# Performance work log

Hardware: AMD Instinct MI355X
Metric: run time of the kernel (lower is better)

The kernel has to match this reference:

```python
import jax, jax.numpy as jnp
import numpy as np

_EPS = 1e-08
SEG = 1024
HOP = 256
PAD = SEG // 2

# periodic Hann window, matching torch.hann_window(SEG) (periodic=True default)
_WINDOW = 0.5 * (1.0 - np.cos(2.0 * np.pi * np.arange(SEG) / SEG))


def setup_inputs() -> dict:
    key = jax.random.key(0)
    k1, k2 = jax.random.split(key)
    B, T = 32, 480000
    estimate = jax.random.normal(k1, (B, T), dtype=jnp.float32)
    target = jax.random.normal(k2, (B, T), dtype=jnp.float32)
    return {"estimate": estimate, "target": target}


def _frame(x):
    # x: [B, T_padded] -> [B, n_frames, SEG] overlapping frames (hop=HOP)
    n_frames = (x.shape[1] - SEG) // HOP + 1
    idx = np.arange(n_frames)[:, None] * HOP + np.arange(SEG)[None, :]
    return x[:, idx]


def reference(estimate, target):
    # zero-mean per utterance
    tgt = target - jnp.mean(target, axis=1, keepdims=True)
    est = estimate - jnp.mean(estimate, axis=1, keepdims=True)
    # centering: reflect-pad SEG//2 on both sides
    tgt = jnp.pad(tgt, ((0, 0), (PAD, PAD)), mode="reflect")
    est = jnp.pad(est, ((0, 0), (PAD, PAD)), mode="reflect")
    # overlapping frames + Hann windowing
    w = jnp.asarray(_WINDOW, dtype=tgt.dtype)  # [SEG]
    T_f = _frame(tgt) * w  # [B, F, SEG]
    E_f = _frame(est) * w  # [B, F, SEG]
    # SI-SDR per segment
    dot = jnp.sum(E_f * T_f, axis=2, keepdims=True)
    s_target_energy = jnp.sum(T_f * T_f, axis=2, keepdims=True) + _EPS
    scaled_target = dot * T_f / s_target_energy
    e_noise = E_f - scaled_target
    ratio = jnp.sum(scaled_target * scaled_target, axis=2) / (
        jnp.sum(e_noise * e_noise, axis=2) + _EPS
    )
    losses = -10.0 * jnp.log10(ratio + _EPS)  # [B, F]
    return losses
```

## Files before the change

### kernel.cpp

```cpp
#include <hip/hip_runtime.h>

#define NB 32
#define TLEN 480000
#define NF 1876
#define FR 4
#define WPR 469
#define NWAVE (WPR * NB)
#define WTHREADS 256

template <int CTRL>
__device__ __forceinline__ float dpp_add(float x) {
    int y = __builtin_amdgcn_update_dpp(0, __float_as_int(x), CTRL, 0xF, 0xF, true);
    return x + __int_as_float(y);
}

__device__ __forceinline__ float wave_reduce(float s) {
    s = dpp_add<0xB1>(s);
    s = dpp_add<0x4E>(s);
    s = dpp_add<0x124>(s);
    s = dpp_add<0x128>(s);
    s += __shfl_xor(s, 16);
    s += __shfl_xor(s, 32);
    return s;
}

__device__ __forceinline__ float f4c(const float4& v, int j) {
    return j == 0 ? v.x : (j == 1 ? v.y : (j == 2 ? v.z : v.w));
}

__device__ __forceinline__ float w2fast(float p) {
    float w = 0.5f - 0.5f * __cosf(p * (6.28318530717958647692f / 1024.0f));
    return w * w;
}

__global__ __launch_bounds__(WTHREADS) void seg_frames(
    const float* __restrict__ est, const float* __restrict__ tgt,
    float* __restrict__ ws_part, float* __restrict__ ws_bs)
{
    const int tid  = threadIdx.x;
    const int lane = tid & 63;
    const int wave = tid >> 6;

    const int gw0 = (blockIdx.x & 7) * (NWAVE / 8) + (blockIdx.x >> 3) * 4;
    const int gw  = gw0 + wave;
    const int b   = gw / WPR;
    const int wv  = gw % WPR;
    const int fb  = wv * FR;

    const float* erow = est + (size_t)b * TLEN;
    const float* trow = tgt + (size_t)b * TLEN;

    float pe = 0.f, pt = 0.f;

    if (fb >= 4 && fb <= 1868) {
        const float4* e4 = (const float4*)erow;
        const float4* t4 = (const float4*)trow;

        float4 E[7], T[7];
#pragma unroll
        for (int m = 0; m < 7; ++m) {
            int g = 64 * (fb + m) - 128 + lane;
            E[m] = e4[g];
            T[m] = t4[g];
        }
        __builtin_amdgcn_sched_barrier(0);

        float w2v[4][4];
#pragma unroll
        for (int q = 0; q < 4; ++q)
#pragma unroll
            for (int j = 0; j < 4; ++j)
                w2v[q][j] = w2fast((float)(256 * q + 4 * lane + j));

        float acc[4][5];
#pragma unroll
        for (int i = 0; i < 4; ++i)
#pragma unroll
            for (int s5 = 0; s5 < 5; ++s5) acc[i][s5] = 0.f;

#pragma unroll
        for (int m = 0; m < 7; ++m) {
            float4 ev4 = E[m], tv4 = T[m];
#pragma unroll
            for (int j = 0; j < 4; ++j) {
                float e = f4c(ev4, j), t = f4c(tv4, j);
                float et = e * t, tt2 = t * t, ee2 = e * e;
#pragma unroll
                for (int i = 0; i < 4; ++i) {
                    if (m - i < 0 || m - i > 3) continue;
                    float w2 = w2v[m - i][j];
                    acc[i][0] = fmaf(w2, et,  acc[i][0]);
                    acc[i][1] = fmaf(w2, tt2, acc[i][1]);
                    acc[i][2] = fmaf(w2, ee2, acc[i][2]);
                    acc[i][3] = fmaf(w2, e,   acc[i][3]);
                    acc[i][4] = fmaf(w2, t,   acc[i][4]);
                }
            }
            if (m < 4) {
                pe += (ev4.x + ev4.y) + (ev4.z + ev4.w);
                pt += (tv4.x + tv4.y) + (tv4.z + tv4.w);
            }
        }

#pragma unroll
        for (int i = 0; i < 4; ++i) {
            float s0 = wave_reduce(acc[i][0]);
            float s1 = wave_reduce(acc[i][1]);
            float s2 = wave_reduce(acc[i][2]);
            float s3 = wave_reduce(acc[i][3]);
            float s4 = wave_reduce(acc[i][4]);
            if (lane == 0) {
                float* p = ws_part + (size_t)(b * NF + fb + i) * 5;
                p[0] = s0; p[1] = s1; p[2] = s2; p[3] = s3; p[4] = s4;
            }
        }
    } else {
        int nfr = NF - fb;
        if (nfr > FR) nfr = FR;

        float w2v[4][4];
#pragma unroll
        for (int q = 0; q < 4; ++q)
#pragma unroll
            for (int j = 0; j < 4; ++j)
                w2v[q][j] = w2fast((float)(256 * q + 4 * lane + j));

        for (int i = 0; i < nfr; ++i) {
            int f = fb + i;
            float s_et = 0.f, s_tt = 0.f, s_ee = 0.f, s_e = 0.f, s_t = 0.f;
#pragma unroll
            for (int q = 0; q < 4; ++q)
#pragma unroll
                for (int j = 0; j < 4; ++j) {
                    int s = 256 * f - 512 + 256 * q + 4 * lane + j;
                    int idx = s < 0 ? -s : (s >= TLEN ? 2 * (TLEN - 1) - s : s);
                    float ev = erow[idx], tv = trow[idx];
                    float w2 = w2v[q][j];
                    float et = ev * tv;
                    s_et = fmaf(w2, et,      s_et);
                    s_tt = fmaf(w2, tv * tv, s_tt);
                    s_ee = fmaf(w2, ev * ev, s_ee);
                    s_e  = fmaf(w2, ev, s_e);
                    s_t  = fmaf(w2, tv, s_t);
                }
            s_et = wave_reduce(s_et);
            s_tt = wave_reduce(s_tt);
            s_ee = wave_reduce(s_ee);
            s_e  = wave_reduce(s_e);
            s_t  = wave_reduce(s_t);
            if (lane == 0) {
                float* p = ws_part + (size_t)(b * NF + f) * 5;
                p[0] = s_et; p[1] = s_tt; p[2] = s_ee; p[3] = s_e; p[4] = s_t;
            }
        }

        const float4* e4 = (const float4*)erow;
        const float4* t4 = (const float4*)trow;
        if (fb == 0) {
#pragma unroll
            for (int k = 0; k < 2; ++k) {
                float4 ev4 = e4[lane + 64 * k];
                float4 tv4 = t4[lane + 64 * k];
                pe += (ev4.x + ev4.y) + (ev4.z + ev4.w);
                pt += (tv4.x + tv4.y) + (tv4.z + tv4.w);
            }
        } else {
#pragma unroll
            for (int k = 0; k < 5; ++k) {
                int g = 119680 + lane + 64 * k;
                float4 ev4 = e4[g];
                float4 tv4 = t4[g];
                pe += (ev4.x + ev4.y) + (ev4.z + ev4.w);
                pt += (tv4.x + tv4.y) + (tv4.z + tv4.w);
            }
        }
    }

    pe = wave_reduce(pe);
    pt = wave_reduce(pt);
    if (lane == 0) {
        ws_bs[(0 * NB + b) * WPR + wv] = pe;
        ws_bs[(1 * NB + b) * WPR + wv] = pt;
    }
}

__global__ __launch_bounds__(WTHREADS) void seg_final(
    const float* __restrict__ ws_part, const float* __restrict__ ws_bs,
    float* __restrict__ out)
{
    const int tid  = threadIdx.x;
    const int lane = tid & 63;
    const int wave = tid >> 6;
    const int idx0 = blockIdx.x * WTHREADS;

    int b0 = idx0 / NF;
    int ilast = idx0 + WTHREADS - 1;
    if (ilast > NB * NF - 1) ilast = NB * NF - 1;
    int b1 = ilast / NF;

    __shared__ float smean[4];
    {
        int sig = wave & 1;
        int row = (wave >> 1) ? b1 : b0;
        const float* pbs = ws_bs + (size_t)(sig * NB + row) * WPR;
        float s = 0.f;
        for (int c = lane; c < WPR; c += 64) s += pbs[c];
        s = wave_reduce(s);
        if (lane == 0) smean[wave] = s * (1.0f / (float)TLEN);
    }
    __syncthreads();

    int idx = idx0 + tid;
    if (idx >= NB * NF) return;
    int b = idx / NF;
    int which = (b == b0) ? 0 : 1;
    float me = smean[which * 2 + 0];
    float mt = smean[which * 2 + 1];

    const float* p = ws_part + (size_t)idx * 5;
    float S_et = p[0], S_tt = p[1], S_ee = p[2], S_e = p[3], S_t = p[4];
    const float W2 = 384.0f;

    float dot = S_et - mt * S_e - me * S_t + me * mt * W2;
    float tt  = S_tt - 2.0f * mt * S_t + mt * mt * W2;
    float ee  = S_ee - 2.0f * me * S_e + me * me * W2;

    float a     = dot / (tt + 1e-8f);
    float st2   = a * a * tt;
    float en2   = ee - 2.0f * a * dot + st2;
    float ratio = st2 / (en2 + 1e-8f);
    out[idx] = -10.0f * log10f(ratio + 1e-8f);
}

extern "C" void kernel_launch(void* const* d_in, const int* in_sizes, int n_in,
                              void* d_out, int out_size, void* d_ws, size_t ws_size,
                              hipStream_t stream)
{
    const float* est = (const float*)d_in[0];
    const float* tgt = (const float*)d_in[1];
    float* out = (float*)d_out;

    float* ws      = (float*)d_ws;
    float* ws_part = ws;
    float* ws_bs   = ws_part + (size_t)NB * NF * 5;

    seg_frames<<<NWAVE / 4, WTHREADS, 0, stream>>>(est, tgt, ws_part, ws_bs);
    dim3 grid2((NB * NF + WTHREADS - 1) / WTHREADS);
    seg_final<<<grid2, WTHREADS, 0, stream>>>(ws_part, ws_bs, out);
}
```

Baseline: 34.40 us.

## Load each hop block once per wave and split frame partials across two buffers

Each wave now reads only its own 4 hop-blocks (4 float4 per lane instead of 7) and adds each block's contributions to the 7 frames that overlap it. Partial sums for frames shared with the neighbouring wave go into separate lo/hi workspace arrays, which the final kernel adds together. This removes the redundant overlapped global loads. The window values come from one sin/cos pair using Hann symmetry, and the wave reduction uses DPP row broadcasts plus readlane in place of shuffles. In exchange each wave does more reductions and stores (7 frames instead of 4), and the final kernel reads twice as much workspace.

Result: slower. 35.09 us (+2.0%).

```diff
diff --git a/kernel.cpp b/kernel.cpp
--- a/kernel.cpp
+++ b/kernel.cpp
@@ -3,8 +3,7 @@
 #define NB 32
 #define TLEN 480000
 #define NF 1876
-#define FR 4
-#define WPR 469
+#define WPR 470
 #define NWAVE (WPR * NB)
 #define WTHREADS 256
 
@@ -19,23 +18,19 @@
     s = dpp_add<0x4E>(s);
     s = dpp_add<0x124>(s);
     s = dpp_add<0x128>(s);
-    s += __shfl_xor(s, 16);
-    s += __shfl_xor(s, 32);
-    return s;
+    s = dpp_add<0x142>(s);
+    s = dpp_add<0x143>(s);
+    return __int_as_float(__builtin_amdgcn_readlane(__float_as_int(s), 63));
 }
 
 __device__ __forceinline__ float f4c(const float4& v, int j) {
     return j == 0 ? v.x : (j == 1 ? v.y : (j == 2 ? v.z : v.w));
 }
 
-__device__ __forceinline__ float w2fast(float p) {
-    float w = 0.5f - 0.5f * __cosf(p * (6.28318530717958647692f / 1024.0f));
-    return w * w;
-}
-
 __global__ __launch_bounds__(WTHREADS) void seg_frames(
     const float* __restrict__ est, const float* __restrict__ tgt,
-    float* __restrict__ ws_part, float* __restrict__ ws_bs)
+    float* __restrict__ ws_lo, float* __restrict__ ws_hi,
+    float* __restrict__ ws_bs)
 {
     const int tid  = threadIdx.x;
     const int lane = tid & 63;
@@ -45,134 +40,109 @@
     const int gw  = gw0 + wave;
     const int b   = gw / WPR;
     const int wv  = gw % WPR;
-    const int fb  = wv * FR;
 
     const float* erow = est + (size_t)b * TLEN;
     const float* trow = tgt + (size_t)b * TLEN;
 
+    float w2v[4][4];
+#pragma unroll
+    for (int j = 0; j < 4; ++j) {
+        float ang = (6.28318530717958647692f / 1024.0f) * (float)(4 * lane + j);
+        float c = __cosf(ang), s = __sinf(ang);
+        float w0 = 0.5f - 0.5f * c;
+        float w1 = 0.5f + 0.5f * s;
+        float w2_ = 0.5f + 0.5f * c;
+        float w3 = 0.5f - 0.5f * s;
+        w2v[0][j] = w0 * w0;
+        w2v[1][j] = w1 * w1;
+        w2v[2][j] = w2_ * w2_;
+        w2v[3][j] = w3 * w3;
+    }
+
+    float acc[7][5];
+#pragma unroll
+    for (int df = 0; df < 7; ++df)
+#pragma unroll
+        for (int s5 = 0; s5 < 5; ++s5) acc[df][s5] = 0.f;
+
     float pe = 0.f, pt = 0.f;
 
-    if (fb >= 4 && fb <= 1868) {
+    if (wv >= 1 && wv <= 468) {
         const float4* e4 = (const float4*)erow;
         const float4* t4 = (const float4*)trow;
 
-        float4 E[7], T[7];
-#pragma unroll
-        for (int m = 0; m < 7; ++m) {
-            int g = 64 * (fb + m) - 128 + lane;
-            E[m] = e4[g];
-            T[m] = t4[g];
+        float4 E[4], T[4];
+#pragma unroll
+        for (int u = 0; u < 4; ++u) {
+            int g4 = 64 * (4 * wv - 2 + u) + lane;
+            E[u] = e4[g4];
+            T[u] = t4[g4];
         }
         __builtin_amdgcn_sched_barrier(0);
 
-        float w2v[4][4];
-#pragma unroll
-        for (int q = 0; q < 4; ++q)
-#pragma unroll
-            for (int j = 0; j < 4; ++j)
-                w2v[q][j] = w2fast((float)(256 * q + 4 * lane + j));
-
-        float acc[4][5];
-#pragma unroll
-        for (int i = 0; i < 4; ++i)
-#pragma unroll
-            for (int s5 = 0; s5 < 5; ++s5) acc[i][s5] = 0.f;
-
-#pragma unroll
-        for (int m = 0; m < 7; ++m) {
-            float4 ev4 = E[m], tv4 = T[m];
+#pragma unroll
+        for (int u = 0; u < 4; ++u) {
+            float4 ev4 = E[u], tv4 = T[u];
 #pragma unroll
             for (int j = 0; j < 4; ++j) {
                 float e = f4c(ev4, j), t = f4c(tv4, j);
                 float et = e * t, tt2 = t * t, ee2 = e * e;
 #pragma unroll
-                for (int i = 0; i < 4; ++i) {
-                    if (m - i < 0 || m - i > 3) continue;
-                    float w2 = w2v[m - i][j];
-                    acc[i][0] = fmaf(w2, et,  acc[i][0]);
-                    acc[i][1] = fmaf(w2, tt2, acc[i][1]);
-                    acc[i][2] = fmaf(w2, ee2, acc[i][2]);
-                    acc[i][3] = fmaf(w2, e,   acc[i][3]);
-                    acc[i][4] = fmaf(w2, t,   acc[i][4]);
+                for (int q = 0; q < 4; ++q) {
+                    const int df = u - q + 3;
+                    float w2 = w2v[q][j];
+                    acc[df][0] = fmaf(w2, et,  acc[df][0]);
+                    acc[df][1] = fmaf(w2, tt2, acc[df][1]);
+                    acc[df][2] = fmaf(w2, ee2, acc[df][2]);
+                    acc[df][3] = fmaf(w2, e,   acc[df][3]);
+                    acc[df][4] = fmaf(w2, t,   acc[df][4]);
                 }
             }
-            if (m < 4) {
-                pe += (ev4.x + ev4.y) + (ev4.z + ev4.w);
-                pt += (tv4.x + tv4.y) + (tv4.z + tv4.w);
+            pe += (ev4.x + ev4.y) + (ev4.z + ev4.w);
+            pt += (tv4.x + tv4.y) + (tv4.z + tv4.w);
+        }
+    } else {
+#pragma unroll
+        for (int u = 0; u < 4; ++u) {
+            int g = 4 * wv - 2 + u;
+            bool ownmean = (wv == 0) ? (u >= 2) : (u == 0);
+#pragma unroll
+            for (int j = 0; j < 4; ++j) {
+                int s = 256 * g + 4 * lane + j;
+                int idx = s < 0 ? -s : (s >= TLEN ? 2 * (TLEN - 1) - s : s);
+                float e = erow[idx], t = trow[idx];
+                float et = e * t, tt2 = t * t, ee2 = e * e;
+#pragma unroll
+                for (int q = 0; q < 4; ++q) {
+                    const int df = u - q + 3;
+                    float w2 = w2v[q][j];
+                    acc[df][0] = fmaf(w2, et,  acc[df][0]);
+                    acc[df][1] = fmaf(w2, tt2, acc[df][1]);
+                    acc[df][2] = fmaf(w2, ee2, acc[df][2]);
+                    acc[df][3] = fmaf(w2, e,   acc[df][3]);
+                    acc[df][4] = fmaf(w2, t,   acc[df][4]);
+                }
+                if (ownmean) { pe += e; pt += t; }
             }
         }
-
-#pragma unroll
-        for (int i = 0; i < 4; ++i) {
-            float s0 = wave_reduce(acc[i][0]);
-            float s1 = wave_reduce(acc[i][1]);
-            float s2 = wave_reduce(acc[i][2]);
-            float s3 = wave_reduce(acc[i][3]);
-            float s4 = wave_reduce(acc[i][4]);
-            if (lane == 0) {
-                float* p = ws_part + (size_t)(b * NF + fb + i) * 5;
-                p[0] = s0; p[1] = s1; p[2] = s2; p[3] = s3; p[4] = s4;
-            }
-        }
-    } else {
-        int nfr = NF - fb;
-        if (nfr > FR) nfr = FR;
-
-        float w2v[4][4];
-#pragma unroll
-        for (int q = 0; q < 4; ++q)
-#pragma unroll
-            for (int j = 0; j < 4; ++j)
-                w2v[q][j] = w2fast((float)(256 * q + 4 * lane + j));
-
-        for (int i = 0; i < nfr; ++i) {
-            int f = fb + i;
-            float s_et = 0.f, s_tt = 0.f, s_ee = 0.f, s_e = 0.f, s_t = 0.f;
-#pragma unroll
-            for (int q = 0; q < 4; ++q)
-#pragma unroll
-                for (int j = 0; j < 4; ++j) {
-                    int s = 256 * f - 512 + 256 * q + 4 * lane + j;
-                    int idx = s < 0 ? -s : (s >= TLEN ? 2 * (TLEN - 1) - s : s);
-                    float ev = erow[idx], tv = trow[idx];
-                    float w2 = w2v[q][j];
-                    float et = ev * tv;
-                    s_et = fmaf(w2, et,      s_et);
-                    s_tt = fmaf(w2, tv * tv, s_tt);
-                    s_ee = fmaf(w2, ev * ev, s_ee);
-                    s_e  = fmaf(w2, ev, s_e);
-                    s_t  = fmaf(w2, tv, s_t);
-                }
-            s_et = wave_reduce(s_et);
-            s_tt = wave_reduce(s_tt);
-            s_ee = wave_reduce(s_ee);
-            s_e  = wave_reduce(s_e);
-            s_t  = wave_reduce(s_t);
-            if (lane == 0) {
-                float* p = ws_part + (size_t)(b * NF + f) * 5;
-                p[0] = s_et; p[1] = s_tt; p[2] = s_ee; p[3] = s_e; p[4] = s_t;
-            }
-        }
-
-        const float4* e4 = (const float4*)erow;
-        const float4* t4 = (const float4*)trow;
-        if (fb == 0) {
-#pragma unroll
-            for (int k = 0; k < 2; ++k) {
-                float4 ev4 = e4[lane + 64 * k];
-                float4 tv4 = t4[lane + 64 * k];
-                pe += (ev4.x + ev4.y) + (ev4.z + ev4.w);
-                pt += (tv4.x + tv4.y) + (tv4.z + tv4.w);
-            }
-        } else {
-#pragma unroll
-            for (int k = 0; k < 5; ++k) {
-                int g = 119680 + lane + 64 * k;
-                float4 ev4 = e4[g];
-                float4 tv4 = t4[g];
-                pe += (ev4.x + ev4.y) + (ev4.z + ev4.w);
-                pt += (tv4.x + tv4.y) + (tv4.z + tv4.w);
-            }
+    }
+
+#pragma unroll
+    for (int df = 0; df < 7; ++df) {
+        const int f = 4 * wv + df - 3;
+        if (f >= 0 && f < NF) {
+            float r0 = wave_reduce(acc[df][0]);
+            float r1 = wave_reduce(acc[df][1]);
+            float r2 = wave_reduce(acc[df][2]);
+            float r3 = wave_reduce(acc[df][3]);
+            float r4 = wave_reduce(acc[df][4]);
+            float v = r0;
+            v = (lane == 1) ? r1 : v;
+            v = (lane == 2) ? r2 : v;
+            v = (lane == 3) ? r3 : v;
+            v = (lane == 4) ? r4 : v;
+            float* dst = (df < 3 ? ws_hi : ws_lo) + (size_t)(b * NF + f) * 5;
+            if (lane < 5) dst[lane] = v;
         }
     }
 
@@ -185,8 +155,8 @@
 }
 
 __global__ __launch_bounds__(WTHREADS) void seg_final(
-    const float* __restrict__ ws_part, const float* __restrict__ ws_bs,
-    float* __restrict__ out)
+    const float* __restrict__ ws_lo, const float* __restrict__ ws_hi,
+    const float* __restrict__ ws_bs, float* __restrict__ out)
 {
     const int tid  = threadIdx.x;
     const int lane = tid & 63;
@@ -213,12 +183,19 @@
     int idx = idx0 + tid;
     if (idx >= NB * NF) return;
     int b = idx / NF;
+    int f = idx - b * NF;
     int which = (b == b0) ? 0 : 1;
     float me = smean[which * 2 + 0];
     float mt = smean[which * 2 + 1];
 
-    const float* p = ws_part + (size_t)idx * 5;
-    float S_et = p[0], S_tt = p[1], S_ee = p[2], S_e = p[3], S_t = p[4];
+    const float* plo = ws_lo + (size_t)idx * 5;
+    const float* phi = ws_hi + (size_t)idx * 5;
+    bool two = (f & 3) != 0;
+    float S_et = plo[0] + (two ? phi[0] : 0.f);
+    float S_tt = plo[1] + (two ? phi[1] : 0.f);
+    float S_ee = plo[2] + (two ? phi[2] : 0.f);
+    float S_e  = plo[3] + (two ? phi[3] : 0.f);
+    float S_t  = plo[4] + (two ? phi[4] : 0.f);
     const float W2 = 384.0f;
 
     float dot = S_et - mt * S_e - me * S_t + me * mt * W2;
@@ -240,11 +217,12 @@
     const float* tgt = (const float*)d_in[1];
     float* out = (float*)d_out;
 
-    float* ws      = (float*)d_ws;
-    float* ws_part = ws;
-    float* ws_bs   = ws_part + (size_t)NB * NF * 5;
-
-    seg_frames<<<NWAVE / 4, WTHREADS, 0, stream>>>(est, tgt, ws_part, ws_bs);
+    float* ws    = (float*)d_ws;
+    float* ws_lo = ws;
+    float* ws_hi = ws_lo + (size_t)NB * NF * 5;
+    float* ws_bs = ws_hi + (size_t)NB * NF * 5;
+
+    seg_frames<<<NWAVE / 4, WTHREADS, 0, stream>>>(est, tgt, ws_lo, ws_hi, ws_bs);
     dim3 grid2((NB * NF + WTHREADS - 1) / WTHREADS);
-    seg_final<<<grid2, WTHREADS, 0, stream>>>(ws_part, ws_bs, out);
-}
+    seg_final<<<grid2, WTHREADS, 0, stream>>>(ws_lo, ws_hi, ws_bs, out);
+}
```
